# Kernel optimization log

Measured on AMD Instinct MI355X. Metric: run time of the kernel, lower is better.

Reference implementation:

```python
import math
import jax, jax.numpy as jnp
import numpy as np

NHEAD = 8


def setup_inputs() -> dict:
    key = jax.random.key(0)
    ks = jax.random.split(key, 16)
    B, S, M, Ss, Ksn, D = 8, 512, 8, 16, 16, 512
    f32 = jnp.float32
    w_scale = 0.05
    return {
        "q_temporal": jax.random.normal(ks[0], (B, S, M, D), f32),
        "k_temporal": jax.random.normal(ks[1], (B, S, M, D), f32),
        "v_temporal": jax.random.normal(ks[2], (B, S, M, D), f32),
        "q_static": jax.random.normal(ks[3], (B, Ss, D), f32),
        "k_static": jax.random.normal(ks[4], (B, Ksn, D), f32),
        "v_static": jax.random.normal(ks[5], (B, Ksn, D), f32),
        "mask_temporal": jax.random.randint(ks[6], (B, S, M), 0, 2).astype(jnp.int32),
        "mask_static": jax.random.randint(ks[7], (B, Ksn), 0, 2).astype(jnp.int32),
        "Wq": jax.random.normal(ks[8], (D, D), f32) * w_scale,
        "bq": jax.random.normal(ks[9], (D,), f32) * w_scale,
        "Wk": jax.random.normal(ks[10], (D, D), f32) * w_scale,
        "bk": jax.random.normal(ks[11], (D,), f32) * w_scale,
        "Wv": jax.random.normal(ks[12], (D, D), f32) * w_scale,
        "bv": jax.random.normal(ks[13], (D,), f32) * w_scale,
        "Wo": jax.random.normal(ks[14], (D, D), f32) * w_scale,
        "bo": jax.random.normal(ks[15], (D,), f32) * w_scale,
    }


def reference(q_temporal, k_temporal, v_temporal, q_static, k_static, v_static,
              mask_temporal, mask_static, Wq, bq, Wk, bk, Wv, bv, Wo, bo):
    B, S, M, D = q_temporal.shape
    dh = D // NHEAD
    scale = 1.0 / math.sqrt(dh)
    SM = S * M

    def lin(x, W, b):
        return x @ W + b

    def h5(x):  # [B,S,M,D] -> [B,H,S,M,dh]
        b, s, m, d = x.shape
        return x.reshape(b, s, m, NHEAD, dh).transpose(0, 3, 1, 2, 4)

    def h4(x):  # [B,N,D] -> [B,H,N,dh]
        b, n, d = x.shape
        return x.reshape(b, n, NHEAD, dh).transpose(0, 2, 1, 3)

    # additive masks: 1 -> 0 (keep), 0 -> -inf
    m_t = jnp.where(mask_temporal == 1, 0.0, -jnp.inf)  # [B,S,M]
    m_s = jnp.where(mask_static == 1, 0.0, -jnp.inf)    # [B,Ks]

    # shared static-key/value heads: [B,H,Ks,dh]
    Ks_h = h4(lin(k_static, Wk, bk))
    Vs_h = h4(lin(v_static, Wv, bv))

    # ---- temporal side ----
    Qt = h5(lin(q_temporal, Wq, bq))   # [B,H,S,M,dh]
    Kt = h5(lin(k_temporal, Wk, bk))
    Vt = h5(lin(v_temporal, Wv, bv))
    qt_kt = jnp.einsum('bhsmd,bhsnd->bhsmn', Qt, Kt) * scale + m_t[:, None, :, None, :]   # [B,H,S,M,M]
    qt_ks = jnp.einsum('bhsmd,bhkd->bhsmk', Qt, Ks_h) * scale + m_s[:, None, None, None, :]  # [B,H,S,M,Ks]
    w_t = jax.nn.softmax(jnp.concatenate([qt_kt, qt_ks], axis=-1), axis=-1)  # [B,H,S,M,M+Ks]
    qkv_t = (jnp.einsum('bhsmn,bhsnd->bhsmd', w_t[..., :M], Vt)
             + jnp.einsum('bhsmk,bhkd->bhsmd', w_t[..., M:], Vs_h))          # [B,H,S,M,dh]
    out_t = lin(qkv_t.transpose(0, 2, 3, 1, 4).reshape(B, S, M, D), Wo, bo)  # [B,S,M,D]

    # ---- static side ----
    Qs = h4(lin(q_static, Wq, bq))                              # [B,H,Ss,dh]
    Kt_f = h4(lin(k_temporal.reshape(B, SM, D), Wk, bk))        # [B,H,S*M,dh]
    Vt_f = h4(lin(v_temporal.reshape(B, SM, D), Wv, bv))
    qs_kt = jnp.einsum('bhqd,bhnd->bhqn', Qs, Kt_f) * scale + m_t.reshape(B, 1, 1, SM)  # [B,H,Ss,S*M]
    qs_ks = jnp.einsum('bhqd,bhkd->bhqk', Qs, Ks_h) * scale + m_s[:, None, None, :]     # [B,H,Ss,Ks]
    w_s = jax.nn.softmax(jnp.concatenate([qs_kt, qs_ks], axis=-1), axis=-1)  # [B,H,Ss,S*M+Ks]
    qkv_s = (jnp.einsum('bhqn,bhnd->bhqd', w_s[..., :SM], Vt_f)
             + jnp.einsum('bhqk,bhkd->bhqd', w_s[..., SM:], Vs_h))           # [B,H,Ss,dh]
    Ss = qkv_s.shape[2]
    out_s = lin(qkv_s.transpose(0, 2, 1, 3).reshape(B, Ss, D), Wo, bo)       # [B,Ss,D]

    return (out_t, w_t, out_s, w_s)
```

## Files before the change

kernel.cpp:

```cpp
#include <hip/hip_runtime.h>
#include <hip/hip_bf16.h>

typedef __attribute__((ext_vector_type(8))) __bf16 bf16x8;
typedef __attribute__((ext_vector_type(4))) float f32x4;

__device__ __forceinline__ float b2f(unsigned short u) {
    unsigned int x = ((unsigned int)u) << 16;
    float f;
    __builtin_memcpy(&f, &x, 4);
    return f;
}
__device__ __forceinline__ unsigned short f2b(float f) {
    __hip_bfloat16 h = __float2bfloat16(f);
    unsigned short u;
    __builtin_memcpy(&u, &h, 2);
    return u;
}
union U4 { uint4 v; unsigned short u[8]; };

__global__ __launch_bounds__(256) void transpose512cvt(const float* __restrict__ in,
                                                       unsigned short* __restrict__ out)
{
    __shared__ float tile[32][33];
    int tx = threadIdx.x & 31, ty = threadIdx.x >> 5;
    int bx = blockIdx.x, by = blockIdx.y;
    #pragma unroll
    for (int i = 0; i < 32; i += 8)
        tile[ty + i][tx] = in[(size_t)(bx * 32 + ty + i) * 512 + by * 32 + tx];
    __syncthreads();
    #pragma unroll
    for (int i = 0; i < 32; i += 8)
        out[(size_t)(by * 32 + ty + i) * 512 + bx * 32 + tx] = f2b(tile[tx][ty + i]);
}

#define GPAD 40

template<bool AF32, int CMODE>
__global__ __launch_bounds__(256) void gemm128(
    const void* __restrict__ Av,
    const unsigned short* __restrict__ Bt,
    const float* __restrict__ bias,
    void* __restrict__ Cv,
    int M, int N)
{
    const int K = 512;
    __shared__ __align__(16) unsigned short As[128 * GPAD];
    __shared__ __align__(16) unsigned short Bs[128 * GPAD];
    int m0 = blockIdx.x * 128, n0 = blockIdx.y * 128;
    int t = threadIdx.x;
    int wave = t >> 6, lane = t & 63, quad = lane >> 4, l16 = lane & 15;
    int wr = wave >> 1, wc = wave & 1;

    f32x4 acc[4][4];
    #pragma unroll
    for (int i = 0; i < 4; ++i)
        #pragma unroll
        for (int j = 0; j < 4; ++j) acc[i][j] = (f32x4){0.f, 0.f, 0.f, 0.f};

    int r = t >> 1, half = (t & 1) * 16;

    for (int k0 = 0; k0 < K; k0 += 32) {
        U4 a0, a1;
        uint4 b0, b1;
        if constexpr (AF32) {
            const float* Ap = (const float*)Av + (size_t)(m0 + r) * K + k0 + half;
            float4 f0 = ((const float4*)Ap)[0], f1 = ((const float4*)Ap)[1];
            float4 f2 = ((const float4*)Ap)[2], f3 = ((const float4*)Ap)[3];
            a0.u[0]=f2b(f0.x); a0.u[1]=f2b(f0.y); a0.u[2]=f2b(f0.z); a0.u[3]=f2b(f0.w);
            a0.u[4]=f2b(f1.x); a0.u[5]=f2b(f1.y); a0.u[6]=f2b(f1.z); a0.u[7]=f2b(f1.w);
            a1.u[0]=f2b(f2.x); a1.u[1]=f2b(f2.y); a1.u[2]=f2b(f2.z); a1.u[3]=f2b(f2.w);
            a1.u[4]=f2b(f3.x); a1.u[5]=f2b(f3.y); a1.u[6]=f2b(f3.z); a1.u[7]=f2b(f3.w);
        } else {
            const unsigned short* Ap = (const unsigned short*)Av + (size_t)(m0 + r) * K + k0 + half;
            a0.v = ((const uint4*)Ap)[0];
            a1.v = ((const uint4*)Ap)[1];
        }
        {
            const unsigned short* Bp = Bt + (size_t)(n0 + r) * K + k0 + half;
            b0 = ((const uint4*)Bp)[0];
            b1 = ((const uint4*)Bp)[1];
        }
        __syncthreads();
        *(uint4*)&As[r * GPAD + half] = a0.v;
        *(uint4*)&As[r * GPAD + half + 8] = a1.v;
        *(uint4*)&Bs[r * GPAD + half] = b0;
        *(uint4*)&Bs[r * GPAD + half + 8] = b1;
        __syncthreads();
        bf16x8 af[4], bf[4];
        #pragma unroll
        for (int i = 0; i < 4; ++i)
            af[i] = *(const bf16x8*)&As[(wr * 64 + i * 16 + l16) * GPAD + quad * 8];
        #pragma unroll
        for (int j = 0; j < 4; ++j)
            bf[j] = *(const bf16x8*)&Bs[(wc * 64 + j * 16 + l16) * GPAD + quad * 8];
        #pragma unroll
        for (int i = 0; i < 4; ++i)
            #pragma unroll
            for (int j = 0; j < 4; ++j)
                acc[i][j] = __builtin_amdgcn_mfma_f32_16x16x32_bf16(af[i], bf[j], acc[i][j], 0, 0, 0);
    }
    #pragma unroll
    for (int i = 0; i < 4; ++i) {
        #pragma unroll
        for (int j = 0; j < 4; ++j) {
            int row = m0 + wr * 64 + i * 16 + quad * 4;
            int col = n0 + wc * 64 + j * 16 + l16;
            float bc = bias[col];
            #pragma unroll
            for (int ii = 0; ii < 4; ++ii) {
                float v = acc[i][j][ii] + bc;
                int R = row + ii;
                if constexpr (CMODE == 0) {
                    ((float*)Cv)[(size_t)R * N + col] = v;
                } else if constexpr (CMODE == 1) {
                    ((unsigned short*)Cv)[(size_t)R * N + col] = f2b(v);
                } else {
                    int bb = R >> 12, n = R & 4095, hh = col >> 6, d = col & 63;
                    ((unsigned short*)Cv)[(((size_t)bb * 8 + hh) * 4096 + n) * 64 + d] = f2b(v);
                }
            }
        }
    }
}

__global__ __launch_bounds__(256) void temporal_attn(
    const unsigned short* __restrict__ Qt, const unsigned short* __restrict__ KH,
    const unsigned short* __restrict__ VH, const unsigned short* __restrict__ Ksp,
    const unsigned short* __restrict__ Vsp,
    const int* __restrict__ mask_t, const int* __restrict__ mask_s,
    float* __restrict__ w_t_out, unsigned short* __restrict__ qkv_t)
{
    int bs = blockIdx.x;
    int b = bs >> 9, s = bs & 511;
    __shared__ __align__(16) unsigned short sK2[64 * 72];
    __shared__ __align__(16) unsigned short sKs[16 * 520];
    __shared__ float wbuf[64 * 24];
    __shared__ float maskadd[24];
    int t = threadIdx.x;

    for (int idx = t; idx < 512; idx += 256) {
        int h = idx >> 6, rem = idx & 63;
        int m = rem >> 3, part = rem & 7;
        uint4 v = *(const uint4*)(KH + ((((size_t)b * 8 + h) * 4096) + s * 8 + m) * 64 + part * 8);
        *(uint4*)&sK2[(h * 8 + m) * 72 + part * 8] = v;
    }
    const uint4* Ksg = (const uint4*)(Ksp + (size_t)b * 8192);
    for (int idx = t; idx < 1024; idx += 256) {
        uint4 v = Ksg[idx];
        *(uint4*)&sKs[(idx >> 6) * 520 + (idx & 63) * 8] = v;
    }
    if (t < 8) maskadd[t] = mask_t[bs * 8 + t] ? 0.f : -1e30f;
    else if (t < 24) maskadd[t] = mask_s[b * 16 + (t - 8)] ? 0.f : -1e30f;

    int p = t >> 2, j = t & 3;
    int h = p >> 3, m = p & 7;

    float qreg[64];
    {
        const uint4* qp = (const uint4*)(Qt + (size_t)bs * 4096 + (size_t)m * 512 + h * 64);
        #pragma unroll
        for (int i = 0; i < 8; ++i) {
            U4 u; u.v = qp[i];
            #pragma unroll
            for (int k = 0; k < 8; ++k) qreg[i * 8 + k] = b2f(u.u[k]);
        }
    }
    __syncthreads();

    float sc[6];
    #pragma unroll
    for (int i = 0; i < 6; ++i) {
        int n = j + i * 4;
        const unsigned short* krow = (n < 8) ? &sK2[(h * 8 + n) * 72] : &sKs[(n - 8) * 520 + h * 64];
        float acc = 0.f;
        #pragma unroll
        for (int d = 0; d < 64; ++d) acc += qreg[d] * b2f(krow[d]);
        sc[i] = acc * 0.125f + maskadd[n];
    }
    float mx = sc[0];
    #pragma unroll
    for (int i = 1; i < 6; ++i) mx = fmaxf(mx, sc[i]);
    mx = fmaxf(mx, __shfl_xor(mx, 1));
    mx = fmaxf(mx, __shfl_xor(mx, 2));
    float e[6], se = 0.f;
    #pragma unroll
    for (int i = 0; i < 6; ++i) { e[i] = __expf(sc[i] - mx); se += e[i]; }
    se += __shfl_xor(se, 1);
    se += __shfl_xor(se, 2);
    float inv = 1.f / se;
    size_t wtb = ((((size_t)b * 8 + h) * 512 + s) * 8 + m) * 24;
    #pragma unroll
    for (int i = 0; i < 6; ++i) {
        int n = j + i * 4;
        float w = e[i] * inv;
        wbuf[p * 24 + n] = w;
        w_t_out[wtb + n] = w;
    }
    __syncthreads();

    int hm = t >> 2, dc = t & 3;
    int h2 = hm >> 3, m2 = hm & 7, d0 = dc * 16;
    float acc2[16];
    #pragma unroll
    for (int i = 0; i < 16; ++i) acc2[i] = 0.f;
    const unsigned short* Vb = VH + (((size_t)(b * 8 + h2)) * 4096 + s * 8) * 64 + d0;
    #pragma unroll
    for (int n = 0; n < 8; ++n) {
        float wv = wbuf[hm * 24 + n];
        U4 a, c;
        a.v = *(const uint4*)(Vb + n * 64);
        c.v = *(const uint4*)(Vb + n * 64 + 8);
        #pragma unroll
        for (int i = 0; i < 8; ++i) { acc2[i] += wv * b2f(a.u[i]); acc2[8 + i] += wv * b2f(c.u[i]); }
    }
    const unsigned short* Vsb = Vsp + (size_t)b * 8192 + h2 * 64 + d0;
    #pragma unroll
    for (int n = 0; n < 16; ++n) {
        float wv = wbuf[hm * 24 + 8 + n];
        U4 a, c;
        a.v = *(const uint4*)(Vsb + n * 512);
        c.v = *(const uint4*)(Vsb + n * 512 + 8);
        #pragma unroll
        for (int i = 0; i < 8; ++i) { acc2[i] += wv * b2f(a.u[i]); acc2[8 + i] += wv * b2f(c.u[i]); }
    }
    unsigned short* op = qkv_t + (size_t)bs * 4096 + (size_t)m2 * 512 + h2 * 64 + d0;
    #pragma unroll
    for (int i = 0; i < 16; ++i) op[i] = f2b(acc2[i]);
}

__global__ __launch_bounds__(256) void static_attn_s1(
    const unsigned short* __restrict__ Qsp, const unsigned short* __restrict__ KH,
    const unsigned short* __restrict__ VH, const unsigned short* __restrict__ Ksp,
    const unsigned short* __restrict__ Vsp,
    const int* __restrict__ mask_t, const int* __restrict__ mask_s,
    float* __restrict__ w_s, float* __restrict__ Ppart, float* __restrict__ Lpart)
{
    int blk = blockIdx.x;
    int bh = blk & 63, c = blk >> 6;
    int b = bh >> 3, h = bh & 7;
    __shared__ __align__(16) unsigned short Klds[32 * 72];
    __shared__ __align__(16) unsigned short Vlds[64 * 40];
    __shared__ __align__(16) unsigned short Plds[16 * 40];
    __shared__ float maskv[32];
    __shared__ float sL[2][16];
    int t = threadIdx.x, wave = t >> 6, lane = t & 63, quad = lane >> 4, l16 = lane & 15;

    bf16x8 qf0 = *(const bf16x8*)(Qsp + ((size_t)(b * 16 + l16)) * 512 + h * 64 + quad * 8);
    bf16x8 qf1 = *(const bf16x8*)(Qsp + ((size_t)(b * 16 + l16)) * 512 + h * 64 + 32 + quad * 8);

    f32x4 pacc = (f32x4){0.f, 0.f, 0.f, 0.f};
    float Lacc[4] = {0.f, 0.f, 0.f, 0.f};
    int d0 = wave * 16;
    int sub = wave >> 1;
    int sr = t >> 3, spart = t & 7;
    int s0 = c * 16, s1 = (c == 7) ? 129 : (s0 + 16);

    for (int st = s0; st < s1; ++st) {
        int key0 = st * 32;
        int kk = key0 + sr;
        uint4 kv = {0, 0, 0, 0}, vv = {0, 0, 0, 0};
        if (kk < 4096) {
            kv = *(const uint4*)(KH + (((size_t)bh) * 4096 + kk) * 64 + spart * 8);
            vv = *(const uint4*)(VH + (((size_t)bh) * 4096 + kk) * 64 + spart * 8);
        } else if (kk < 4112) {
            kv = *(const uint4*)(Ksp + ((size_t)(b * 16 + kk - 4096)) * 512 + h * 64 + spart * 8);
            vv = *(const uint4*)(Vsp + ((size_t)(b * 16 + kk - 4096)) * 512 + h * 64 + spart * 8);
        }
        __syncthreads();
        *(uint4*)&Klds[sr * 72 + spart * 8] = kv;
        {
            U4 u; u.v = vv;
            #pragma unroll
            for (int ii = 0; ii < 8; ++ii) Vlds[(spart * 8 + ii) * 40 + sr] = u.u[ii];
        }
        if (t < 32) {
            int k2 = key0 + t;
            float ma = -1e30f;
            if (k2 < 4096) ma = mask_t[b * 4096 + k2] ? 0.f : -1e30f;
            else if (k2 < 4112) ma = mask_s[b * 16 + k2 - 4096] ? 0.f : -1e30f;
            maskv[t] = ma;
        }
        __syncthreads();
        if ((wave & 1) == 0) {
            bf16x8 kf0 = *(const bf16x8*)&Klds[(sub * 16 + l16) * 72 + quad * 8];
            bf16x8 kf1 = *(const bf16x8*)&Klds[(sub * 16 + l16) * 72 + 32 + quad * 8];
            f32x4 sc = (f32x4){0.f, 0.f, 0.f, 0.f};
            sc = __builtin_amdgcn_mfma_f32_16x16x32_bf16(qf0, kf0, sc, 0, 0, 0);
            sc = __builtin_amdgcn_mfma_f32_16x16x32_bf16(qf1, kf1, sc, 0, 0, 0);
            float ma = maskv[sub * 16 + l16];
            size_t wbase = (((size_t)bh) * 16 + quad * 4) * 4112 + key0 + sub * 16 + l16;
            #pragma unroll
            for (int i = 0; i < 4; ++i) {
                float sv = sc[i] * 0.125f + ma;
                float w = __expf(sv);
                Lacc[i] += w;
                w_s[wbase + (size_t)i * 4112] = w;
                Plds[(quad * 4 + i) * 40 + sub * 16 + l16] = f2b(w);
            }
        }
        __syncthreads();
        bf16x8 pf = *(const bf16x8*)&Plds[l16 * 40 + quad * 8];
        bf16x8 vf = *(const bf16x8*)&Vlds[(d0 + l16) * 40 + quad * 8];
        pacc = __builtin_amdgcn_mfma_f32_16x16x32_bf16(pf, vf, pacc, 0, 0, 0);
    }

    if ((wave & 1) == 0) {
        #pragma unroll
        for (int i = 0; i < 4; ++i) {
            float v = Lacc[i];
            v += __shfl_xor(v, 1);
            v += __shfl_xor(v, 2);
            v += __shfl_xor(v, 4);
            v += __shfl_xor(v, 8);
            Lacc[i] = v;
        }
        if (l16 == 0) {
            #pragma unroll
            for (int i = 0; i < 4; ++i) sL[wave >> 1][quad * 4 + i] = Lacc[i];
        }
    }
    size_t pbase = ((size_t)(bh * 8 + c) * 16 + quad * 4) * 64 + d0 + l16;
    #pragma unroll
    for (int i = 0; i < 4; ++i) Ppart[pbase + (size_t)i * 64] = pacc[i];
    __syncthreads();
    if (t < 16) Lpart[(bh * 8 + c) * 16 + t] = sL[0][t] + sL[1][t];
}

__global__ __launch_bounds__(256) void static_attn_s4(
    const float* __restrict__ Ppart, const float* __restrict__ Lpart,
    float* __restrict__ w_s, unsigned short* __restrict__ qkvS)
{
    int bh = blockIdx.x, b = bh >> 3, h = bh & 7;
    __shared__ float invL[16];
    int t = threadIdx.x;
    if (t < 16) {
        float L = 0.f;
        #pragma unroll
        for (int cc = 0; cc < 8; ++cc) L += Lpart[(bh * 8 + cc) * 16 + t];
        invL[t] = 1.f / L;
    }
    __syncthreads();
    #pragma unroll
    for (int i = 0; i < 4; ++i) {
        int idx = t + i * 256;
        int q = idx >> 6, d = idx & 63;
        float s = 0.f;
        #pragma unroll
        for (int cc = 0; cc < 8; ++cc) s += Ppart[((size_t)(bh * 8 + cc) * 16 + q) * 64 + d];
        qkvS[((size_t)(b * 16 + q)) * 512 + h * 64 + d] = f2b(s * invL[q]);
    }
    size_t base = (size_t)bh * 16 * 4112;
    for (int q = 0; q < 16; ++q) {
        float il = invL[q];
        for (int kk = t; kk < 4112; kk += 256) w_s[base + q * 4112 + kk] *= il;
    }
}

extern "C" void kernel_launch(void* const* d_in, const int* in_sizes, int n_in,
                              void* d_out, int out_size, void* d_ws, size_t ws_size,
                              hipStream_t stream)
{
    const float* q_t = (const float*)d_in[0];
    const float* k_t = (const float*)d_in[1];
    const float* v_t = (const float*)d_in[2];
    const float* q_s = (const float*)d_in[3];
    const float* k_s = (const float*)d_in[4];
    const float* v_s = (const float*)d_in[5];
    const int* m_t = (const int*)d_in[6];
    const int* m_s = (const int*)d_in[7];
    const float* Wq = (const float*)d_in[8];
    const float* bq = (const float*)d_in[9];
    const float* Wk = (const float*)d_in[10];
    const float* bk = (const float*)d_in[11];
    const float* Wv = (const float*)d_in[12];
    const float* bv = (const float*)d_in[13];
    const float* Wo = (const float*)d_in[14];
    const float* bo = (const float*)d_in[15];

    char* ws = (char*)d_ws;
    size_t off = 0;
    auto alloc = [&](size_t bytes) {
        void* p = ws + off;
        off += (bytes + 255) & ~(size_t)255;
        return p;
    };
    const size_t WB = (size_t)512 * 512 * 2;
    const size_t TB = (size_t)32768 * 512 * 2;
    const size_t SB = (size_t)128 * 512 * 2;
    unsigned short* WqT = (unsigned short*)alloc(WB);
    unsigned short* WkT = (unsigned short*)alloc(WB);
    unsigned short* WvT = (unsigned short*)alloc(WB);
    unsigned short* WoT = (unsigned short*)alloc(WB);
    unsigned short* Qt   = (unsigned short*)alloc(TB);
    unsigned short* KH   = (unsigned short*)alloc(TB);
    unsigned short* VH   = (unsigned short*)alloc(TB);
    unsigned short* qkvT = (unsigned short*)alloc(TB);
    unsigned short* Qsp  = (unsigned short*)alloc(SB);
    unsigned short* Ksp  = (unsigned short*)alloc(SB);
    unsigned short* Vsp  = (unsigned short*)alloc(SB);
    unsigned short* qkvS = (unsigned short*)alloc(SB);
    float* Ppart = (float*)alloc((size_t)64 * 8 * 16 * 64 * 4);
    float* Lpart = (float*)alloc((size_t)64 * 8 * 16 * 4);

    float* out    = (float*)d_out;
    float* out_tp = out;
    float* w_t_o  = out + 16777216;
    float* out_sp = out + 23068672;
    float* w_s_o  = out + 23134208;

    transpose512cvt<<<dim3(16, 16), 256, 0, stream>>>(Wq, WqT);
    transpose512cvt<<<dim3(16, 16), 256, 0, stream>>>(Wk, WkT);
    transpose512cvt<<<dim3(16, 16), 256, 0, stream>>>(Wv, WvT);
    transpose512cvt<<<dim3(16, 16), 256, 0, stream>>>(Wo, WoT);

    gemm128<true, 1><<<dim3(256, 4), 256, 0, stream>>>(q_t, WqT, bq, Qt, 32768, 512);
    gemm128<true, 2><<<dim3(256, 4), 256, 0, stream>>>(k_t, WkT, bk, KH, 32768, 512);
    gemm128<true, 2><<<dim3(256, 4), 256, 0, stream>>>(v_t, WvT, bv, VH, 32768, 512);
    gemm128<true, 1><<<dim3(1, 4),   256, 0, stream>>>(q_s, WqT, bq, Qsp, 128, 512);
    gemm128<true, 1><<<dim3(1, 4),   256, 0, stream>>>(k_s, WkT, bk, Ksp, 128, 512);
    gemm128<true, 1><<<dim3(1, 4),   256, 0, stream>>>(v_s, WvT, bv, Vsp, 128, 512);

    temporal_attn<<<4096, 256, 0, stream>>>(Qt, KH, VH, Ksp, Vsp, m_t, m_s, w_t_o, qkvT);
    static_attn_s1<<<512, 256, 0, stream>>>(Qsp, KH, VH, Ksp, Vsp, m_t, m_s, w_s_o, Ppart, Lpart);
    static_attn_s4<<<64, 256, 0, stream>>>(Ppart, Lpart, w_s_o, qkvS);

    gemm128<false, 0><<<dim3(256, 4), 256, 0, stream>>>(qkvT, WoT, bo, out_tp, 32768, 512);
    gemm128<false, 0><<<dim3(1, 4),   256, 0, stream>>>(qkvS, WoT, bo, out_sp, 128, 512);
}
```

Before: 620.6 us.

## Rewrite temporal attention with MFMA over two timesteps per block

The temporal attention kernel now processes two sequence positions per block, with one wave per head. QK scores and PV products are computed with bf16 16x16x32 MFMA instructions instead of scalar FMA loops. A block-diagonal validity mask stops each timestep's queries from attending to the other timestep's keys. V is transposed into LDS per wave, and the probabilities are staged in LDS as bf16 for the PV MFMA. This removes the heavy per-thread scalar dot products, at the cost of bf16 rounding of the softmax weights and scattered scalar stores for w_t and qkv_t.

```diff
diff --git a/kernel.cpp b/kernel.cpp
--- a/kernel.cpp
+++ b/kernel.cpp
@@ -123,109 +123,111 @@
     }
 }
 
-__global__ __launch_bounds__(256) void temporal_attn(
+__global__ __launch_bounds__(512) void temporal_attn(
     const unsigned short* __restrict__ Qt, const unsigned short* __restrict__ KH,
     const unsigned short* __restrict__ VH, const unsigned short* __restrict__ Ksp,
     const unsigned short* __restrict__ Vsp,
     const int* __restrict__ mask_t, const int* __restrict__ mask_s,
     float* __restrict__ w_t_out, unsigned short* __restrict__ qkv_t)
 {
-    int bs = blockIdx.x;
-    int b = bs >> 9, s = bs & 511;
-    __shared__ __align__(16) unsigned short sK2[64 * 72];
-    __shared__ __align__(16) unsigned short sKs[16 * 520];
-    __shared__ float wbuf[64 * 24];
-    __shared__ float maskadd[24];
+    int blk = blockIdx.x;
+    int b = blk >> 8, sp = blk & 255;
+    int s0 = sp * 2;
     int t = threadIdx.x;
-
-    for (int idx = t; idx < 512; idx += 256) {
-        int h = idx >> 6, rem = idx & 63;
-        int m = rem >> 3, part = rem & 7;
-        uint4 v = *(const uint4*)(KH + ((((size_t)b * 8 + h) * 4096) + s * 8 + m) * 64 + part * 8);
-        *(uint4*)&sK2[(h * 8 + m) * 72 + part * 8] = v;
-    }
-    const uint4* Ksg = (const uint4*)(Ksp + (size_t)b * 8192);
-    for (int idx = t; idx < 1024; idx += 256) {
-        uint4 v = Ksg[idx];
-        *(uint4*)&sKs[(idx >> 6) * 520 + (idx & 63) * 8] = v;
-    }
-    if (t < 8) maskadd[t] = mask_t[bs * 8 + t] ? 0.f : -1e30f;
-    else if (t < 24) maskadd[t] = mask_s[b * 16 + (t - 8)] ? 0.f : -1e30f;
-
-    int p = t >> 2, j = t & 3;
-    int h = p >> 3, m = p & 7;
-
-    float qreg[64];
+    int h = t >> 6, lane = t & 63, quad = lane >> 4, l16 = lane & 15;
+
+    __shared__ __align__(16) unsigned short Vt[8][64 * 40];
+    __shared__ __align__(16) unsigned short Pl[8][16 * 40];
+
+    size_t bh = (size_t)(b * 8 + h);
+    size_t tok0 = ((size_t)(b * 512 + s0)) * 8;
+
     {
-        const uint4* qp = (const uint4*)(Qt + (size_t)bs * 4096 + (size_t)m * 512 + h * 64);
-        #pragma unroll
-        for (int i = 0; i < 8; ++i) {
-            U4 u; u.v = qp[i];
-            #pragma unroll
-            for (int k = 0; k < 8; ++k) qreg[i * 8 + k] = b2f(u.u[k]);
-        }
-    }
-    __syncthreads();
-
-    float sc[6];
-    #pragma unroll
-    for (int i = 0; i < 6; ++i) {
-        int n = j + i * 4;
-        const unsigned short* krow = (n < 8) ? &sK2[(h * 8 + n) * 72] : &sKs[(n - 8) * 520 + h * 64];
-        float acc = 0.f;
-        #pragma unroll
-        for (int d = 0; d < 64; ++d) acc += qreg[d] * b2f(krow[d]);
-        sc[i] = acc * 0.125f + maskadd[n];
-    }
-    float mx = sc[0];
-    #pragma unroll
-    for (int i = 1; i < 6; ++i) mx = fmaxf(mx, sc[i]);
-    mx = fmaxf(mx, __shfl_xor(mx, 1));
-    mx = fmaxf(mx, __shfl_xor(mx, 2));
-    float e[6], se = 0.f;
-    #pragma unroll
-    for (int i = 0; i < 6; ++i) { e[i] = __expf(sc[i] - mx); se += e[i]; }
-    se += __shfl_xor(se, 1);
-    se += __shfl_xor(se, 2);
-    float inv = 1.f / se;
-    size_t wtb = ((((size_t)b * 8 + h) * 512 + s) * 8 + m) * 24;
-    #pragma unroll
-    for (int i = 0; i < 6; ++i) {
-        int n = j + i * 4;
-        float w = e[i] * inv;
-        wbuf[p * 24 + n] = w;
-        w_t_out[wtb + n] = w;
-    }
-    __syncthreads();
-
-    int hm = t >> 2, dc = t & 3;
-    int h2 = hm >> 3, m2 = hm & 7, d0 = dc * 16;
-    float acc2[16];
-    #pragma unroll
-    for (int i = 0; i < 16; ++i) acc2[i] = 0.f;
-    const unsigned short* Vb = VH + (((size_t)(b * 8 + h2)) * 4096 + s * 8) * 64 + d0;
-    #pragma unroll
-    for (int n = 0; n < 8; ++n) {
-        float wv = wbuf[hm * 24 + n];
-        U4 a, c;
-        a.v = *(const uint4*)(Vb + n * 64);
-        c.v = *(const uint4*)(Vb + n * 64 + 8);
-        #pragma unroll
-        for (int i = 0; i < 8; ++i) { acc2[i] += wv * b2f(a.u[i]); acc2[8 + i] += wv * b2f(c.u[i]); }
-    }
-    const unsigned short* Vsb = Vsp + (size_t)b * 8192 + h2 * 64 + d0;
-    #pragma unroll
-    for (int n = 0; n < 16; ++n) {
-        float wv = wbuf[hm * 24 + 8 + n];
-        U4 a, c;
-        a.v = *(const uint4*)(Vsb + n * 512);
-        c.v = *(const uint4*)(Vsb + n * 512 + 8);
-        #pragma unroll
-        for (int i = 0; i < 8; ++i) { acc2[i] += wv * b2f(a.u[i]); acc2[8 + i] += wv * b2f(c.u[i]); }
-    }
-    unsigned short* op = qkv_t + (size_t)bs * 4096 + (size_t)m2 * 512 + h2 * 64 + d0;
-    #pragma unroll
-    for (int i = 0; i < 16; ++i) op[i] = f2b(acc2[i]);
+        int r = lane & 31, dh = (lane >> 5) * 32;
+        const unsigned short* src = (r < 16)
+            ? VH + (bh * 4096 + (size_t)(s0 * 8 + r)) * 64 + dh
+            : Vsp + ((size_t)(b * 16 + (r - 16))) * 512 + h * 64 + dh;
+        U4 u[4];
+        #pragma unroll
+        for (int g = 0; g < 4; ++g) u[g].v = ((const uint4*)src)[g];
+        unsigned short* dst = &Vt[h][0];
+        #pragma unroll
+        for (int g = 0; g < 4; ++g)
+            #pragma unroll
+            for (int ii = 0; ii < 8; ++ii)
+                dst[(dh + g * 8 + ii) * 40 + r] = u[g].u[ii];
+    }
+
+    const unsigned short* qp = Qt + (tok0 + l16) * 512 + h * 64 + quad * 8;
+    bf16x8 qf0 = *(const bf16x8*)qp;
+    bf16x8 qf1 = *(const bf16x8*)(qp + 32);
+    const unsigned short* kpt = KH + (bh * 4096 + (size_t)(s0 * 8 + l16)) * 64 + quad * 8;
+    bf16x8 kt0 = *(const bf16x8*)kpt;
+    bf16x8 kt1 = *(const bf16x8*)(kpt + 32);
+    const unsigned short* kps = Ksp + ((size_t)(b * 16 + l16)) * 512 + h * 64 + quad * 8;
+    bf16x8 ks0 = *(const bf16x8*)kps;
+    bf16x8 ks1 = *(const bf16x8*)(kps + 32);
+
+    f32x4 sc0 = (f32x4){0.f, 0.f, 0.f, 0.f};
+    f32x4 sc1 = (f32x4){0.f, 0.f, 0.f, 0.f};
+    sc0 = __builtin_amdgcn_mfma_f32_16x16x32_bf16(qf0, kt0, sc0, 0, 0, 0);
+    sc0 = __builtin_amdgcn_mfma_f32_16x16x32_bf16(qf1, kt1, sc0, 0, 0, 0);
+    sc1 = __builtin_amdgcn_mfma_f32_16x16x32_bf16(qf0, ks0, sc1, 0, 0, 0);
+    sc1 = __builtin_amdgcn_mfma_f32_16x16x32_bf16(qf1, ks1, sc1, 0, 0, 0);
+
+    float madd0 = mask_t[tok0 + l16] ? 0.f : -1e30f;
+    bool v0 = ((quad < 2) == (l16 < 8));
+    if (!v0) madd0 = -1e30f;
+    float madd1 = mask_s[b * 16 + l16] ? 0.f : -1e30f;
+
+    float w0[4], w1[4];
+    #pragma unroll
+    for (int i = 0; i < 4; ++i) {
+        float a = sc0[i] * 0.125f + madd0;
+        float c = sc1[i] * 0.125f + madd1;
+        float mx = fmaxf(a, c);
+        mx = fmaxf(mx, __shfl_xor(mx, 1));
+        mx = fmaxf(mx, __shfl_xor(mx, 2));
+        mx = fmaxf(mx, __shfl_xor(mx, 4));
+        mx = fmaxf(mx, __shfl_xor(mx, 8));
+        float e0 = __expf(a - mx), e1 = __expf(c - mx);
+        float se = e0 + e1;
+        se += __shfl_xor(se, 1);
+        se += __shfl_xor(se, 2);
+        se += __shfl_xor(se, 4);
+        se += __shfl_xor(se, 8);
+        float inv = 1.f / se;
+        w0[i] = e0 * inv;
+        w1[i] = e1 * inv;
+    }
+
+    int row0 = quad * 4;
+    #pragma unroll
+    for (int i = 0; i < 4; ++i) {
+        int row = row0 + i;
+        Pl[h][row * 40 + l16] = f2b(w0[i]);
+        Pl[h][row * 40 + 16 + l16] = f2b(w1[i]);
+        int s = s0 + (row >> 3), m = row & 7;
+        size_t wb = ((((size_t)b * 8 + h) * 512 + s) * 8 + m) * 24;
+        if (v0) w_t_out[wb + (l16 & 7)] = w0[i];
+        w_t_out[wb + 8 + l16] = w1[i];
+    }
+
+    bf16x8 pa = *(const bf16x8*)&Pl[h][l16 * 40 + quad * 8];
+    f32x4 oacc[4];
+    #pragma unroll
+    for (int j = 0; j < 4; ++j) {
+        bf16x8 vb = *(const bf16x8*)&Vt[h][(j * 16 + l16) * 40 + quad * 8];
+        oacc[j] = (f32x4){0.f, 0.f, 0.f, 0.f};
+        oacc[j] = __builtin_amdgcn_mfma_f32_16x16x32_bf16(pa, vb, oacc[j], 0, 0, 0);
+    }
+    #pragma unroll
+    for (int j = 0; j < 4; ++j)
+        #pragma unroll
+        for (int ii = 0; ii < 4; ++ii) {
+            int row = quad * 4 + ii;
+            qkv_t[(tok0 + row) * 512 + h * 64 + j * 16 + l16] = f2b(oacc[j][ii]);
+        }
 }
 
 __global__ __launch_bounds__(256) void static_attn_s1(
@@ -420,7 +422,7 @@
     gemm128<true, 1><<<dim3(1, 4),   256, 0, stream>>>(k_s, WkT, bk, Ksp, 128, 512);
     gemm128<true, 1><<<dim3(1, 4),   256, 0, stream>>>(v_s, WvT, bv, Vsp, 128, 512);
 
-    temporal_attn<<<4096, 256, 0, stream>>>(Qt, KH, VH, Ksp, Vsp, m_t, m_s, w_t_o, qkvT);
+    temporal_attn<<<2048, 512, 0, stream>>>(Qt, KH, VH, Ksp, Vsp, m_t, m_s, w_t_o, qkvT);
     static_attn_s1<<<512, 256, 0, stream>>>(Qsp, KH, VH, Ksp, Vsp, m_t, m_s, w_s_o, Ppart, Lpart);
     static_attn_s4<<<64, 256, 0, stream>>>(Ppart, Lpart, w_s_o, qkvS);
 
```

Result: faster. 599.5 us (-3.4%).
